# Optimization experiments

Measured on AMD Instinct MI355X. Metric: run time of the kernel, lower is better.

The kernel has to match this reference:

```python
import math
import jax, jax.numpy as jnp
import numpy as np

T, C, NH = 2048, 1024, 16
HD = C // NH


def setup_inputs() -> dict:
    key = jax.random.key(0)
    ks = jax.random.split(key, 5)
    return {
        "x": jax.random.normal(ks[0], (T, C), dtype=jnp.float32),
        "w_attn": jax.random.normal(ks[1], (3 * C, C), dtype=jnp.float32) * (1.0 / math.sqrt(C)),
        "b_attn": jax.random.normal(ks[2], (3 * C,), dtype=jnp.float32) * 0.02,
        "w_proj": jax.random.normal(ks[3], (C, C), dtype=jnp.float32) * (1.0 / math.sqrt(C)),
        "b_proj": jax.random.normal(ks[4], (C,), dtype=jnp.float32) * 0.02,
    }


def reference(x, w_attn, b_attn, w_proj, b_proj):
    t, c = x.shape
    # qkv projection: eqx Linear computes W @ x + b, vmapped over T
    qkv = x @ w_attn.T + b_attn  # (T, 3C)
    q, k, v = jnp.split(qkv, 3, axis=1)  # each (T, C)
    # (T, NH, HD) -> (NH, T, HD)
    q = jnp.swapaxes(q.reshape(t, NH, HD), 0, 1)
    k = jnp.swapaxes(k.reshape(t, NH, HD), 0, 1)
    v = jnp.swapaxes(v.reshape(t, NH, HD), 0, 1)
    att = jnp.einsum('hqd,hkd->hqk', q, k) / math.sqrt(HD)  # (NH, T, T)
    causal = jnp.tril(jnp.ones((t, t), dtype=bool))
    att = jnp.where(causal[None, :, :], att, -jnp.inf)
    att = jax.nn.softmax(att, axis=-1)
    y = jnp.matmul(att, v)  # (NH, T, HD)
    # Faithful to source: swapaxes(1,2) on (NH, T, HD) -> (NH, HD, T), then reshape
    y = jnp.swapaxes(y, 1, 2).reshape(t, c)
    return y @ w_proj.T + b_proj
```

## Files before the change

kernel.cpp:

```cpp
#include <hip/hip_runtime.h>
#include <hip/hip_bf16.h>
#include <stdint.h>

typedef __bf16 bf16;
typedef __bf16 bf16x8 __attribute__((ext_vector_type(8)));
typedef __bf16 bf16x4 __attribute__((ext_vector_type(4)));
typedef float floatx4 __attribute__((ext_vector_type(4)));
typedef short short4v __attribute__((ext_vector_type(4)));

#define T_DIM 2048
#define C_DIM 1024
#define NH    16
#define HD    64

__device__ __forceinline__ void gload_lds16(const void* g, void* l) {
    __builtin_amdgcn_global_load_lds(
        (__attribute__((address_space(1))) void*)(g),
        (__attribute__((address_space(3))) void*)(l),
        16, 0, 0);
}

#define MFMA16(a, b, c)  __builtin_amdgcn_mfma_f32_16x16x32_bf16(a, b, c, 0, 0, 0)
#define MFMAK16(a, b, c) __builtin_amdgcn_mfma_f32_16x16x16bf16_1k(a, b, c, 0, 0, 0)

__global__ __launch_bounds__(256) void cvt_all(
    const float* __restrict__ x, const float* __restrict__ wa,
    const float* __restrict__ wp,
    bf16* __restrict__ xb, bf16* __restrict__ wab, bf16* __restrict__ wpb)
{
    const int i = blockIdx.x * 256 + threadIdx.x;
    const float* src; bf16* dst; int off;
    if (i < 262144)      { src = x;  dst = xb;  off = i; }
    else if (i < 655360) { src = wa; dst = wab; off = i - 262144; }
    else                 { src = wp; dst = wpb; off = i - 655360; }
    const float4 a = ((const float4*)src)[off * 2];
    const float4 b = ((const float4*)src)[off * 2 + 1];
    bf16x8 o;
    o[0] = (bf16)a.x; o[1] = (bf16)a.y; o[2] = (bf16)a.z; o[3] = (bf16)a.w;
    o[4] = (bf16)b.x; o[5] = (bf16)b.y; o[6] = (bf16)b.z; o[7] = (bf16)b.w;
    *(bf16x8*)(dst + (size_t)off * 8) = o;
}

template<int MODE, int TM, int TN>
__global__ __launch_bounds__(256) void csa_gemm_bt(
    const bf16* __restrict__ A, const bf16* __restrict__ B,
    const float* __restrict__ bias,
    void* __restrict__ out0v, bf16* __restrict__ out1, bf16* __restrict__ out2)
{
    constexpr int K   = 1024;
    constexpr int WM  = (TM == 128) ? 4 : 2;
    constexpr int WN  = 4 / WM;
    constexpr int MT  = 2;
    constexpr int NT  = TN / (16 * WN);
    constexpr int ACH = TM / 32;
    constexpr int BCH = TN / 32;
    __shared__ __align__(16) bf16 sA[2][TM * 64];
    __shared__ __align__(16) bf16 sB[2][TN * 64];

    const int tid  = threadIdx.x;
    const int lane = tid & 63;
    const int wid  = tid >> 6;
    const int wm   = wid & (WM - 1);
    const int wn   = wid / WM;
    const int rowbase = wm * 32;
    const int colbase = wn * (TN / WN);
    const int tileM = blockIdx.x * TM;
    const int tileN = blockIdx.y * TN;

    const int fr   = lane & 15;
    const int quad = lane >> 4;
    const int f7   = fr & 7;

    auto stage = [&](int b, int k0) {
#pragma unroll
        for (int i = 0; i < ACH; i++) {
            const int cid = tid + 256 * i;
            const int row = cid >> 3, pc = cid & 7;
            gload_lds16(A + (long)(tileM + row) * K + k0 + (pc ^ (row & 7)) * 8,
                        &sA[b][0] + cid * 8);
        }
#pragma unroll
        for (int i = 0; i < BCH; i++) {
            const int cid = tid + 256 * i;
            const int row = cid >> 3, pc = cid & 7;
            gload_lds16(B + (long)(tileN + row) * K + k0 + (pc ^ (row & 7)) * 8,
                        &sB[b][0] + cid * 8);
        }
    };

    floatx4 acc[MT][NT];
#pragma unroll
    for (int i = 0; i < MT; i++)
#pragma unroll
        for (int j = 0; j < NT; j++) acc[i][j] = (floatx4){0.f, 0.f, 0.f, 0.f};

    stage(0, 0);

    for (int it = 0; it < K / 64; ++it) {
        __syncthreads();
        if (it + 1 < K / 64) stage((it + 1) & 1, (it + 1) * 64);
        const bf16* A_ = &sA[it & 1][0];
        const bf16* B_ = &sB[it & 1][0];

        bf16x8 af[MT][2], bfr[NT][2];
#pragma unroll
        for (int mt = 0; mt < MT; mt++) {
            const int row = rowbase + mt * 16 + fr;
#pragma unroll
            for (int kh = 0; kh < 2; kh++)
                af[mt][kh] = *(const bf16x8*)(A_ + row * 64 +
                                              ((kh * 4 + quad) ^ f7) * 8);
        }
#pragma unroll
        for (int nt = 0; nt < NT; nt++) {
            const int row = colbase + nt * 16 + fr;
#pragma unroll
            for (int kh = 0; kh < 2; kh++)
                bfr[nt][kh] = *(const bf16x8*)(B_ + row * 64 +
                                               ((kh * 4 + quad) ^ f7) * 8);
        }
#pragma unroll
        for (int mt = 0; mt < MT; mt++)
#pragma unroll
            for (int nt = 0; nt < NT; nt++) {
                acc[mt][nt] = MFMA16(af[mt][0], bfr[nt][0], acc[mt][nt]);
                acc[mt][nt] = MFMA16(af[mt][1], bfr[nt][1], acc[mt][nt]);
            }
    }

#pragma unroll
    for (int mt = 0; mt < MT; mt++) {
#pragma unroll
        for (int nt = 0; nt < NT; nt++) {
            const int gn = tileN + colbase + nt * 16 + fr;
            const float bv = bias[gn];
            const int gmb = tileM + rowbase + mt * 16 + quad * 4;
            if (MODE == 0) {
                const int which = gn >> 10;
                const int w2 = gn & 1023;
                const int hh = w2 >> 6, d = w2 & 63;
                if (which == 2) {
                    bf16x4 pk;
#pragma unroll
                    for (int r = 0; r < 4; r++) pk[r] = (bf16)(acc[mt][nt][r] + bv);
                    *(bf16x4*)(out2 + ((long)(hh * HD + d) << 11) + gmb) = pk;
                } else {
                    bf16* dst = (which == 0) ? (bf16*)out0v : out1;
#pragma unroll
                    for (int r = 0; r < 4; r++)
                        dst[((long)hh * T_DIM + gmb + r) * HD + d] =
                            (bf16)(acc[mt][nt][r] + bv);
                }
            } else {
#pragma unroll
                for (int r = 0; r < 4; r++)
                    ((float*)out0v)[(long)(gmb + r) * C_DIM + gn] =
                        acc[mt][nt][r] + bv;
            }
        }
    }
}

__global__ __launch_bounds__(256) void csa_attn_chunk(
    const bf16* __restrict__ Qh, const bf16* __restrict__ Kh,
    const bf16* __restrict__ Vth, float* __restrict__ Opart,
    float* __restrict__ lpart, bf16* __restrict__ YY)
{
    __shared__ __align__(16) bf16 sK[2][64 * 64];
    __shared__ __align__(16) bf16 sV[2][64 * 64];

    const int c  = blockIdx.x;
    const int h  = blockIdx.y;
    const int qt = 31 - (int)blockIdx.z;
    const int nk = qt + 1;
    const int kt0 = c * 8;
    if (kt0 >= nk) return;
    const int ktend = (kt0 + 8 < nk) ? kt0 + 8 : nk;

    const int tid  = threadIdx.x;
    const int lane = tid & 63;
    const int wid  = tid >> 6;
    const int fr   = lane & 15;
    const int quad = lane >> 4;
    const int f7   = fr & 7;
    const int q0   = qt * 64;
    const int qg   = q0 + wid * 16 + fr;

    const bf16* qrow = Qh + ((long)h * T_DIM + qg) * HD;
    const bf16x8 qf0 = *(const bf16x8*)(qrow + quad * 8);
    const bf16x8 qf1 = *(const bf16x8*)(qrow + quad * 8 + 32);

    const int rb   = tid >> 3;
    const int cswz = (tid & 7) ^ (rb & 7);

    auto stage = [&](int b, int k0) {
        gload_lds16(Kh + ((long)(h * T_DIM + k0 + rb) << 6) + cswz * 8,
                    &sK[b][0] + tid * 8);
        gload_lds16(Kh + ((long)(h * T_DIM + k0 + rb + 32) << 6) + cswz * 8,
                    &sK[b][0] + 2048 + tid * 8);
        gload_lds16(Vth + ((long)(h * HD + rb) << 11) + k0 + cswz * 8,
                    &sV[b][0] + tid * 8);
        gload_lds16(Vth + ((long)(h * HD + rb + 32) << 11) + k0 + cswz * 8,
                    &sV[b][0] + 2048 + tid * 8);
    };

    stage(0, kt0 * 64);

    float l_i = 0.f;
    floatx4 o_acc[4];
#pragma unroll
    for (int d4 = 0; d4 < 4; d4++) o_acc[d4] = (floatx4){0.f, 0.f, 0.f, 0.f};

    for (int kt = kt0; kt < ktend; ++kt) {
        const int it = kt - kt0;
        __syncthreads();
        if (kt + 1 < ktend) stage((it + 1) & 1, (kt + 1) * 64);
        const bf16* K_ = &sK[it & 1][0];
        const bf16* V_ = &sV[it & 1][0];
        const int k0 = kt * 64;
        const bool diag = (kt == qt);

        short4v pa[4];
        float s = 0.f;
#pragma unroll
        for (int nt = 0; nt < 4; nt++) {
            const bf16* kr = K_ + (nt * 16 + fr) * 64;
            const bf16x8 ka0 = *(const bf16x8*)(kr + (quad ^ f7) * 8);
            const bf16x8 ka1 = *(const bf16x8*)(kr + ((quad + 4) ^ f7) * 8);
            floatx4 z = (floatx4){0.f, 0.f, 0.f, 0.f};
            z = MFMA16(ka0, qf0, z);
            z = MFMA16(ka1, qf1, z);
            const int kgb = k0 + nt * 16 + quad * 4;
            bf16x4 pk;
#pragma unroll
            for (int r = 0; r < 4; r++) {
                const float e = __builtin_amdgcn_exp2f(z[r] * 0.1803368801f);
                const float pv = (!diag || (kgb + r <= qg)) ? e : 0.f;
                s += pv;
                pk[r] = (bf16)pv;
            }
            pa[nt] = __builtin_bit_cast(short4v, pk);
        }
        s += __shfl_xor(s, 16);
        s += __shfl_xor(s, 32);
        l_i += s;

#pragma unroll
        for (int d4 = 0; d4 < 4; d4++) {
            const bf16* vrow = V_ + (d4 * 16 + fr) * 64;
#pragma unroll
            for (int nt = 0; nt < 4; nt++) {
                const short4v vb = __builtin_bit_cast(short4v,
                    *(const bf16x4*)(vrow +
                        (((2 * nt + (quad >> 1)) ^ f7) * 8) + (quad & 1) * 4));
                o_acc[d4] = MFMAK16(pa[nt], vb, o_acc[d4]);
            }
        }
    }

    if (kt0 == 0 && ktend == nk) {
        const float inv_self = 1.f / l_i;
        float inv[4];
#pragma unroll
        for (int r = 0; r < 4; r++) inv[r] = __shfl(inv_self, quad * 4 + r);
#pragma unroll
        for (int r = 0; r < 4; r++) {
            const int q = q0 + wid * 16 + quad * 4 + r;
            const int rq = q >> 10, cq = q & 1023;
#pragma unroll
            for (int d4 = 0; d4 < 4; d4++) {
                const int d = d4 * 16 + fr;
                YY[(long)(h * 128 + 2 * d + rq) * 1024 + cq] =
                    (bf16)(o_acc[d4][r] * inv[r]);
            }
        }
    } else {
        const long obase = ((long)((h * 32 + qt) * 4 + c)) * 4096;
#pragma unroll
        for (int d4 = 0; d4 < 4; d4++)
#pragma unroll
            for (int r = 0; r < 4; r++)
                Opart[obase + (wid * 16 + quad * 4 + r) * 64 + d4 * 16 + fr] =
                    o_acc[d4][r];
        if (quad == 0)
            lpart[((h * 32 + qt) * 4 + c) * 64 + wid * 16 + fr] = l_i;
    }
}

__global__ __launch_bounds__(256) void csa_combine(
    const float* __restrict__ Opart, const float* __restrict__ lpart,
    bf16* __restrict__ YY)
{
    const int qt = blockIdx.x + 8;
    const int h  = blockIdx.y;
    const int nc = (qt >> 3) + 1;
    const int t  = threadIdx.x;
    const int q  = t >> 2;
    const int d0 = (t & 3) * 16;

    const long obase = ((long)((h * 32 + qt) * 4)) * 4096 + q * 64 + d0;
    const int  lbase = (h * 32 + qt) * 4 * 64 + q;

    float4 acc[4] = {};
    float lq = 0.f;
    for (int c = 0; c < nc; c++) {
        const float4* src = (const float4*)(Opart + obase + (long)c * 4096);
#pragma unroll
        for (int j = 0; j < 4; j++) {
            const float4 v = src[j];
            acc[j].x += v.x; acc[j].y += v.y; acc[j].z += v.z; acc[j].w += v.w;
        }
        lq += lpart[lbase + c * 64];
    }
    const float inv = 1.f / lq;
    const int qglob = qt * 64 + q;
    const int rq = qglob >> 10, cq = qglob & 1023;
#pragma unroll
    for (int j = 0; j < 4; j++) {
        const float vv[4] = {acc[j].x, acc[j].y, acc[j].z, acc[j].w};
#pragma unroll
        for (int k = 0; k < 4; k++) {
            const int d = d0 + j * 4 + k;
            YY[(long)(h * 128 + 2 * d + rq) * 1024 + cq] = (bf16)(vv[k] * inv);
        }
    }
}

extern "C" void kernel_launch(void* const* d_in, const int* in_sizes, int n_in,
                              void* d_out, int out_size, void* d_ws, size_t ws_size,
                              hipStream_t stream) {
    (void)in_sizes; (void)n_in; (void)out_size; (void)ws_size;
    const float* x      = (const float*)d_in[0];
    const float* w_attn = (const float*)d_in[1];
    const float* b_attn = (const float*)d_in[2];
    const float* w_proj = (const float*)d_in[3];
    const float* b_proj = (const float*)d_in[4];

    bf16* xb  = (bf16*)d_ws;
    bf16* wab = xb  + (size_t)T_DIM * C_DIM;
    bf16* wpb = wab + (size_t)3 * C_DIM * C_DIM;
    bf16* Q   = wpb + (size_t)C_DIM * C_DIM;
    bf16* Kp  = Q   + (size_t)NH * T_DIM * HD;
    bf16* Vt  = Kp  + (size_t)NH * T_DIM * HD;
    bf16* YY  = Vt  + (size_t)NH * T_DIM * HD;
    float* Opart = (float*)(YY + (size_t)T_DIM * C_DIM);
    float* lpart = Opart + (size_t)16 * 32 * 4 * 4096;

    cvt_all<<<3072, 256, 0, stream>>>(x, w_attn, w_proj, xb, wab, wpb);

    csa_gemm_bt<0, 128, 64><<<dim3(16, 48), 256, 0, stream>>>(xb, wab, b_attn, Q, Kp, Vt);
    csa_attn_chunk<<<dim3(4, NH, 32), 256, 0, stream>>>(Q, Kp, Vt, Opart, lpart, YY);
    csa_combine<<<dim3(24, NH), 256, 0, stream>>>(Opart, lpart, YY);
    csa_gemm_bt<1, 64, 64><<<dim3(32, 16), 256, 0, stream>>>(YY, wpb, b_proj, d_out, nullptr, nullptr);
}
```

Baseline: 153.8 us.

## Use 16x16x32 MFMA for PV via LDS reshuffle of P tile

```diff
diff --git a/kernel.cpp b/kernel.cpp
--- a/kernel.cpp
+++ b/kernel.cpp
@@ -6,7 +6,6 @@
 typedef __bf16 bf16x8 __attribute__((ext_vector_type(8)));
 typedef __bf16 bf16x4 __attribute__((ext_vector_type(4)));
 typedef float floatx4 __attribute__((ext_vector_type(4)));
-typedef short short4v __attribute__((ext_vector_type(4)));
 
 #define T_DIM 2048
 #define C_DIM 1024
@@ -21,7 +20,6 @@
 }
 
 #define MFMA16(a, b, c)  __builtin_amdgcn_mfma_f32_16x16x32_bf16(a, b, c, 0, 0, 0)
-#define MFMAK16(a, b, c) __builtin_amdgcn_mfma_f32_16x16x16bf16_1k(a, b, c, 0, 0, 0)
 
 __global__ __launch_bounds__(256) void cvt_all(
     const float* __restrict__ x, const float* __restrict__ wa,
@@ -168,6 +166,7 @@
 {
     __shared__ __align__(16) bf16 sK[2][64 * 64];
     __shared__ __align__(16) bf16 sV[2][64 * 64];
+    __shared__ __align__(16) bf16 sP[4][16 * 64];
 
     const int c  = blockIdx.x;
     const int h  = blockIdx.y;
@@ -220,8 +219,7 @@
         const int k0 = kt * 64;
         const bool diag = (kt == qt);
 
-        short4v pa[4];
-        float s = 0.f;
+        float p[4][4];
 #pragma unroll
         for (int nt = 0; nt < 4; nt++) {
             const bf16* kr = K_ + (nt * 16 + fr) * 64;
@@ -231,30 +229,42 @@
             z = MFMA16(ka0, qf0, z);
             z = MFMA16(ka1, qf1, z);
             const int kgb = k0 + nt * 16 + quad * 4;
-            bf16x4 pk;
 #pragma unroll
             for (int r = 0; r < 4; r++) {
                 const float e = __builtin_amdgcn_exp2f(z[r] * 0.1803368801f);
-                const float pv = (!diag || (kgb + r <= qg)) ? e : 0.f;
-                s += pv;
-                pk[r] = (bf16)pv;
+                p[nt][r] = (!diag || (kgb + r <= qg)) ? e : 0.f;
             }
-            pa[nt] = __builtin_bit_cast(short4v, pk);
-        }
+        }
+
+        float s = 0.f;
+#pragma unroll
+        for (int nt = 0; nt < 4; nt++)
+#pragma unroll
+            for (int r = 0; r < 4; r++) s += p[nt][r];
         s += __shfl_xor(s, 16);
         s += __shfl_xor(s, 32);
         l_i += s;
 
+        bf16* pw = &sP[wid][0];
+#pragma unroll
+        for (int nt = 0; nt < 4; nt++) {
+            bf16x4 pk;
+#pragma unroll
+            for (int r = 0; r < 4; r++) pk[r] = (bf16)p[nt][r];
+            *(bf16x4*)(pw + fr * 64 +
+                       (((2 * nt + (quad >> 1)) ^ f7) * 8) + (quad & 1) * 4) = pk;
+        }
+        asm volatile("s_waitcnt lgkmcnt(0)" ::: "memory");
+        const bf16x8 pa0 = *(const bf16x8*)(pw + fr * 64 + (quad ^ f7) * 8);
+        const bf16x8 pa1 = *(const bf16x8*)(pw + fr * 64 + ((quad + 4) ^ f7) * 8);
+
 #pragma unroll
         for (int d4 = 0; d4 < 4; d4++) {
-            const bf16* vrow = V_ + (d4 * 16 + fr) * 64;
-#pragma unroll
-            for (int nt = 0; nt < 4; nt++) {
-                const short4v vb = __builtin_bit_cast(short4v,
-                    *(const bf16x4*)(vrow +
-                        (((2 * nt + (quad >> 1)) ^ f7) * 8) + (quad & 1) * 4));
-                o_acc[d4] = MFMAK16(pa[nt], vb, o_acc[d4]);
-            }
+            const bf16* vr = V_ + (d4 * 16 + fr) * 64;
+            const bf16x8 vb0 = *(const bf16x8*)(vr + (quad ^ f7) * 8);
+            const bf16x8 vb1 = *(const bf16x8*)(vr + ((quad + 4) ^ f7) * 8);
+            o_acc[d4] = MFMA16(pa0, vb0, o_acc[d4]);
+            o_acc[d4] = MFMA16(pa1, vb1, o_acc[d4]);
         }
     }
 
```

Measured after the change: 153.6 us. About the same (-0.2%).
